# Performance work log

Measured on AMD Instinct MI355X. Metric: run time of the kernel, lower is better.

## Reference

```python
import jax, jax.numpy as jnp
import numpy as np
from jax import lax

M1 = M2 = M3 = 8  # Fourier modes per axis


def _corners(x):
    # gather the 4 low-frequency corner blocks -> [B, C, 2*M1, 2*M2, M3]
    top = jnp.concatenate([x[:, :, :M1, :M2, :M3], x[:, :, -M1:, :M2, :M3]], axis=2)
    bot = jnp.concatenate([x[:, :, :M1, -M2:, :M3], x[:, :, -M1:, -M2:, :M3]], axis=2)
    return jnp.concatenate([top, bot], axis=3)


def _scatter(template, xm):
    # place the mixed corner blocks back into a zero spectrum shaped like template
    xp = jnp.zeros_like(template)
    xp = xp.at[:, :, :M1, :M2, :M3].set(xm[:, :, :M1, :M2, :M3])
    xp = xp.at[:, :, -M1:, :M2, :M3].set(xm[:, :, -M1:, :M2, :M3])
    xp = xp.at[:, :, :M1, -M2:, :M3].set(xm[:, :, :M1, -M2:, :M3])
    xp = xp.at[:, :, -M1:, -M2:, :M3].set(xm[:, :, -M1:, -M2:, :M3])
    return xp


def _spectral_conv(x, w):
    # x: complex [B,C,X,Y,Zr]; w: real [Ci,Co,16,16,14]
    xm = _corners(x)                                    # [B,C,16,16,8] complex
    xr = jnp.fft.irfftn(xm, axes=(-3, -2, -1))          # [B,C,16,16,14] real
    y = jnp.einsum('bixyz,ioxyz->boxyz', xr, w)         # per-point channel mix
    ym = jnp.fft.rfftn(y, axes=(-3, -2, -1))            # [B,C,16,16,8] complex
    return _scatter(x, ym.astype(x.dtype))


def _cgelu(z):
    # torch: complex(gelu(real), gelu(imag)); F.gelu default is exact erf
    return lax.complex(jax.nn.gelu(z.real, approximate=False),
                       jax.nn.gelu(z.imag, approximate=False))


def _cmix(x, wr, wi):
    # einsum 'bi...,io...->bo...' with [Ci,Co,1,1,1] complex pointwise weight
    return jnp.einsum('bixyz,io->boxyz', x, lax.complex(wr, wi))


def setup_inputs() -> dict:
    key = jax.random.key(0)
    ks = jax.random.split(key, 12)
    B, X, Y, Zr = 4, 64, 64, 33
    W = 20
    inp = {
        'x_r': jax.random.normal(ks[0], (B, 3, X, Y, Zr), jnp.float32),
        'x_i': jax.random.normal(ks[1], (B, 3, X, Y, Zr), jnp.float32),
        'smooth': jax.random.uniform(ks[2], (1, 1, X, Y, Zr), jnp.float32),
        'wconv': 0.001 * jax.random.uniform(ks[3], (4, W, W, 2 * M1, 2 * M2, 2 * M3 - 2), jnp.float32),
        'wpt_r': 0.1 * jax.random.uniform(ks[4], (4, W, W), jnp.float32),
        'wpt_i': 0.1 * jax.random.uniform(ks[5], (4, W, W), jnp.float32),
        'fc0_r': 0.1 * jax.random.uniform(ks[6], (3, W), jnp.float32),
        'fc0_i': 0.1 * jax.random.uniform(ks[7], (3, W), jnp.float32),
        'fc1_r': 0.1 * jax.random.uniform(ks[8], (W, 128), jnp.float32),
        'fc1_i': 0.1 * jax.random.uniform(ks[9], (W, 128), jnp.float32),
        'fc2_r': 0.1 * jax.random.uniform(ks[10], (128, 3), jnp.float32),
        'fc2_i': 0.1 * jax.random.uniform(ks[11], (128, 3), jnp.float32),
    }
    return inp


def reference(x_r, x_i, smooth, wconv, wpt_r, wpt_i, fc0_r, fc0_i,
              fc1_r, fc1_i, fc2_r, fc2_i):
    x = lax.complex(x_r, x_i)                     # [B,3,64,64,33] complex64
    x = _cmix(x, fc0_r, fc0_i)                    # lift to width=20
    for l in range(4):
        x1 = _spectral_conv(x, wconv[l])
        x2 = _cmix(x, wpt_r[l], wpt_i[l])
        x = (x1 + x2) * smooth                    # real smoother broadcast
        if l < 3:
            x = _cgelu(x)
    x = _cmix(x, fc1_r, fc1_i)                    # 20 -> 128
    x = _cgelu(x)
    x = _cmix(x, fc2_r, fc2_i)                    # 128 -> 3
    return x
```

## Files before the change

### kernel.cpp

```cpp
#include <hip/hip_runtime.h>
#include <hip/hip_bf16.h>
#include <math.h>

#define XYZ 135168
#define W 20
#define NMODE 2048
#define NREAL 3584

__device__ __forceinline__ float n22_erf(float x) {
    float s = (x < 0.f) ? -1.f : 1.f;
    float a = fabsf(x);
    float t = 1.f / fmaf(0.3275911f, a, 1.f);
    float poly = t * fmaf(t, fmaf(t, fmaf(t, fmaf(t, 1.061405429f, -1.453152027f),
                                           1.421413741f), -0.284496736f), 0.254829592f);
    float e = __expf(-a * a);
    return s * (1.f - poly * e);
}
__device__ __forceinline__ float n22_gelu(float v) {
    return 0.5f * v * (1.0f + n22_erf(v * 0.7071067811865476f));
}

__global__ __launch_bounds__(256, 4)
void n22_fc0(const float* __restrict__ xr_in, const float* __restrict__ xi_in,
             const float* __restrict__ fr, const float* __restrict__ fi,
             float* __restrict__ xre, float* __restrict__ xim) {
    int idx = blockIdx.x * blockDim.x + threadIdx.x;
    if (idx >= 4 * XYZ) return;
    int b = idx / XYZ, p = idx % XYZ;
    float ar[3], ai[3];
#pragma unroll
    for (int i = 0; i < 3; i++) {
        ar[i] = xr_in[(size_t)(b * 3 + i) * XYZ + p];
        ai[i] = xi_in[(size_t)(b * 3 + i) * XYZ + p];
    }
#pragma unroll
    for (int o = 0; o < W; o++) {
        float rr = 0.f, ii = 0.f;
#pragma unroll
        for (int i = 0; i < 3; i++) {
            float wr = fr[i * W + o], wi = fi[i * W + o];
            rr += ar[i] * wr - ai[i] * wi;
            ii += ar[i] * wi + ai[i] * wr;
        }
        xre[(size_t)(b * W + o) * XYZ + p] = rr;
        xim[(size_t)(b * W + o) * XYZ + p] = ii;
    }
}

__global__ __launch_bounds__(256, 4)
void n22_ixy(const float* __restrict__ xre, const float* __restrict__ xim,
             float* __restrict__ aRe, float* __restrict__ aIm) {
    __shared__ float s0r[256], s0i[256], s1r[256], s1i[256];
    int bc = blockIdx.x >> 3;
    int kz = blockIdx.x & 7;
    int t = threadIdx.x;
    int hi = t >> 4, lo = t & 15;
    {
        int row = (hi < 8) ? hi : hi + 48;
        int col = (lo < 8) ? lo : lo + 48;
        int off = (row * 64 + col) * 33 + kz;
        s0r[t] = xre[(size_t)bc * XYZ + off];
        s0i[t] = xim[(size_t)bc * XYZ + off];
    }
    __syncthreads();
    {
        int nx = hi, ky = lo;
        float accr = 0.f, acci = 0.f;
        for (int kx = 0; kx < 16; kx++) {
            float vr = s0r[kx * 16 + ky], vi = s0i[kx * 16 + ky];
            int m = (kx * nx) & 15;
            float s, c;
            sincosf((float)m * 0.39269908169872414f, &s, &c);
            accr += vr * c - vi * s;
            acci += vr * s + vi * c;
        }
        s1r[t] = accr * 0.0625f;
        s1i[t] = acci * 0.0625f;
    }
    __syncthreads();
    {
        int nx = hi, ny = lo;
        float accr = 0.f, acci = 0.f;
        for (int ky = 0; ky < 16; ky++) {
            float vr = s1r[nx * 16 + ky], vi = s1i[nx * 16 + ky];
            int m = (ky * ny) & 15;
            float s, c;
            sincosf((float)m * 0.39269908169872414f, &s, &c);
            accr += vr * c - vi * s;
            acci += vr * s + vi * c;
        }
        size_t o = (size_t)bc * 2048 + (size_t)t * 8 + kz;
        aRe[o] = accr * 0.0625f;
        aIm[o] = acci * 0.0625f;
    }
}

__global__ __launch_bounds__(256, 4)
void n22_irfftz(const float* __restrict__ aRe, const float* __restrict__ aIm,
                float* __restrict__ r1) {
    int t = blockIdx.x * blockDim.x + threadIdx.x;
    if (t >= 80 * NREAL) return;
    int nz = t % 14;
    int q = t / 14;
    int base = q * 8;
    float acc = aRe[base];
    float re7 = aRe[base + 7];
    acc += (nz & 1) ? -re7 : re7;
    for (int k = 1; k < 7; k++) {
        int m = (k * nz) % 14;
        float s, c;
        sincosf((float)m * 0.4487989505128276f, &s, &c);
        acc += 2.f * (aRe[base + k] * c - aIm[base + k] * s);
    }
    r1[t] = acc * (1.0f / 14.0f);
}

__global__ __launch_bounds__(256, 4)
void n22_mix(const float* __restrict__ r1, const float* __restrict__ wconv,
             int l, float* __restrict__ r2) {
    int t = blockIdx.x * blockDim.x + threadIdx.x;
    if (t >= 80 * NREAL) return;
    int p = t % NREAL;
    int o = (t / NREAL) % W;
    int b = t / (NREAL * W);
    const float* wl = wconv + (size_t)l * W * W * NREAL;
    float acc = 0.f;
#pragma unroll
    for (int i = 0; i < W; i++)
        acc += r1[(size_t)(b * W + i) * NREAL + p] * wl[(size_t)(i * W + o) * NREAL + p];
    r2[t] = acc;
}

__global__ __launch_bounds__(256, 4)
void n22_rfftz(const float* __restrict__ r2,
               float* __restrict__ c1Re, float* __restrict__ c1Im) {
    int t = blockIdx.x * blockDim.x + threadIdx.x;
    if (t >= 80 * NMODE) return;
    int k = t & 7;
    int q = t >> 3;
    int base = q * 14;
    float accr = 0.f, acci = 0.f;
    for (int n = 0; n < 14; n++) {
        float v = r2[base + n];
        int m = (k * n) % 14;
        float s, c;
        sincosf((float)m * 0.4487989505128276f, &s, &c);
        accr += v * c;
        acci -= v * s;
    }
    c1Re[t] = accr;
    c1Im[t] = acci;
}

__global__ __launch_bounds__(256, 4)
void n22_fxy(const float* __restrict__ c1Re, const float* __restrict__ c1Im,
             float* __restrict__ eRe, float* __restrict__ eIm) {
    __shared__ float s0r[256], s0i[256], s1r[256], s1i[256];
    int bc = blockIdx.x >> 3;
    int kz = blockIdx.x & 7;
    int t = threadIdx.x;
    int hi = t >> 4, lo = t & 15;
    {
        size_t o = (size_t)bc * 2048 + (size_t)t * 8 + kz;
        s0r[t] = c1Re[o];
        s0i[t] = c1Im[o];
    }
    __syncthreads();
    {
        int kx = hi, ny = lo;
        float accr = 0.f, acci = 0.f;
        for (int nx = 0; nx < 16; nx++) {
            float vr = s0r[nx * 16 + ny], vi = s0i[nx * 16 + ny];
            int m = (kx * nx) & 15;
            float s, c;
            sincosf((float)m * 0.39269908169872414f, &s, &c);
            accr += vr * c + vi * s;
            acci += vi * c - vr * s;
        }
        s1r[t] = accr;
        s1i[t] = acci;
    }
    __syncthreads();
    {
        int kx = hi, ky = lo;
        float accr = 0.f, acci = 0.f;
        for (int ny = 0; ny < 16; ny++) {
            float vr = s1r[kx * 16 + ny], vi = s1i[kx * 16 + ny];
            int m = (ky * ny) & 15;
            float s, c;
            sincosf((float)m * 0.39269908169872414f, &s, &c);
            accr += vr * c + vi * s;
            acci += vi * c - vr * s;
        }
        size_t o = (size_t)bc * 2048 + (size_t)t * 8 + kz;
        eRe[o] = accr;
        eIm[o] = acci;
    }
}

__global__ __launch_bounds__(256, 4)
void n22_combine(float* __restrict__ xre, float* __restrict__ xim,
                 const float* __restrict__ ere, const float* __restrict__ eim,
                 const float* __restrict__ wpt_r, const float* __restrict__ wpt_i,
                 int l, const float* __restrict__ smooth) {
    __shared__ float wr[W * W], wi[W * W];
    for (int i = threadIdx.x; i < W * W; i += blockDim.x) {
        wr[i] = wpt_r[l * W * W + i];
        wi[i] = wpt_i[l * W * W + i];
    }
    __syncthreads();
    int idx = blockIdx.x * blockDim.x + threadIdx.x;
    if (idx >= 4 * XYZ) return;
    int b = idx / XYZ, p = idx % XYZ;
    int gz = p % 33;
    int gxy = p / 33;
    int gy = gxy & 63;
    int gx = gxy >> 6;
    int kx = (gx < 8) ? gx : ((gx >= 56) ? gx - 48 : -1);
    int ky = (gy < 8) ? gy : ((gy >= 56) ? gy - 48 : -1);
    bool corner = (kx >= 0) && (ky >= 0) && (gz < 8);
    float sm = smooth[p];
    float ar[W], ai[W];
#pragma unroll
    for (int i = 0; i < W; i++) {
        ar[i] = xre[(size_t)(b * W + i) * XYZ + p];
        ai[i] = xim[(size_t)(b * W + i) * XYZ + p];
    }
    int ebase = corner ? (b * W * NMODE + (kx * 16 + ky) * 8 + gz) : 0;
    for (int o = 0; o < W; o++) {
        float rr = 0.f, ii = 0.f;
#pragma unroll
        for (int i = 0; i < W; i++) {
            float wwr = wr[i * W + o], wwi = wi[i * W + o];
            rr += ar[i] * wwr - ai[i] * wwi;
            ii += ar[i] * wwi + ai[i] * wwr;
        }
        if (corner) {
            rr += ere[ebase + o * NMODE];
            ii += eim[ebase + o * NMODE];
        }
        rr *= sm;
        ii *= sm;
        rr = n22_gelu(rr);
        ii = n22_gelu(ii);
        xre[(size_t)(b * W + o) * XYZ + p] = rr;
        xim[(size_t)(b * W + o) * XYZ + p] = ii;
    }
}

__global__ __launch_bounds__(256, 2)
void n22_tail(const float* __restrict__ xre, const float* __restrict__ xim,
              const float* __restrict__ ere, const float* __restrict__ eim,
              const float* __restrict__ wpt_r, const float* __restrict__ wpt_i,
              const float* __restrict__ smooth,
              const float* __restrict__ f1r, const float* __restrict__ f1i,
              const float* __restrict__ f2r, const float* __restrict__ f2i,
              float* __restrict__ outf) {
    __shared__ __align__(16) float w1r[W * 128], w1i[W * 128];
    __shared__ __align__(16) float w2r[3 * 128], w2i[3 * 128];
    __shared__ float pwr[W * W], pwi[W * W];
    for (int i = threadIdx.x; i < W * 128; i += blockDim.x) {
        w1r[i] = f1r[i];
        w1i[i] = f1i[i];
    }
    for (int i = threadIdx.x; i < 3 * 128; i += blockDim.x) {
        int j = i & 127, o = i >> 7;
        w2r[o * 128 + j] = f2r[j * 3 + o];
        w2i[o * 128 + j] = f2i[j * 3 + o];
    }
    for (int i = threadIdx.x; i < W * W; i += blockDim.x) {
        pwr[i] = wpt_r[3 * W * W + i];
        pwi[i] = wpt_i[3 * W * W + i];
    }
    __syncthreads();
    int idx = blockIdx.x * blockDim.x + threadIdx.x;
    if (idx >= 4 * XYZ) return;
    int b = idx / XYZ, p = idx % XYZ;
    int gz = p % 33;
    int gxy = p / 33;
    int gy = gxy & 63;
    int gx = gxy >> 6;
    int kxc = (gx < 8) ? gx : ((gx >= 56) ? gx - 48 : -1);
    int kyc = (gy < 8) ? gy : ((gy >= 56) ? gy - 48 : -1);
    bool corner = (kxc >= 0) && (kyc >= 0) && (gz < 8);
    float sm = smooth[p];
    float rr_[W], ri_[W];
    {
        float ar[W], ai[W];
#pragma unroll
        for (int i = 0; i < W; i++) {
            ar[i] = xre[(size_t)(b * W + i) * XYZ + p];
            ai[i] = xim[(size_t)(b * W + i) * XYZ + p];
        }
        int ebase = corner ? (b * W * NMODE + (kxc * 16 + kyc) * 8 + gz) : 0;
#pragma unroll 1
        for (int o = 0; o < W; o++) {
            float rr = 0.f, ii = 0.f;
#pragma unroll
            for (int i = 0; i < W; i++) {
                float wwr = pwr[i * W + o], wwi = pwi[i * W + o];
                rr += ar[i] * wwr - ai[i] * wwi;
                ii += ar[i] * wwi + ai[i] * wwr;
            }
            if (corner) {
                rr += ere[ebase + o * NMODE];
                ii += eim[ebase + o * NMODE];
            }
            rr_[o] = rr * sm;
            ri_[o] = ii * sm;
        }
    }
    float accr[3] = {0.f, 0.f, 0.f};
    for (int jc = 0; jc < 16; jc++) {
        int jb = jc * 8;
        float tr[8], ti[8];
#pragma unroll
        for (int jj = 0; jj < 8; jj++) { tr[jj] = 0.f; ti[jj] = 0.f; }
#pragma unroll 1
        for (int i = 0; i < W; i++) {
            float4 wrA = *(const float4*)&w1r[i * 128 + jb];
            float4 wrB = *(const float4*)&w1r[i * 128 + jb + 4];
            float4 wiA = *(const float4*)&w1i[i * 128 + jb];
            float4 wiB = *(const float4*)&w1i[i * 128 + jb + 4];
            float xr_ = rr_[i], xi_ = ri_[i];
            tr[0] += xr_ * wrA.x - xi_ * wiA.x;  ti[0] += xr_ * wiA.x + xi_ * wrA.x;
            tr[1] += xr_ * wrA.y - xi_ * wiA.y;  ti[1] += xr_ * wiA.y + xi_ * wrA.y;
            tr[2] += xr_ * wrA.z - xi_ * wiA.z;  ti[2] += xr_ * wiA.z + xi_ * wrA.z;
            tr[3] += xr_ * wrA.w - xi_ * wiA.w;  ti[3] += xr_ * wiA.w + xi_ * wrA.w;
            tr[4] += xr_ * wrB.x - xi_ * wiB.x;  ti[4] += xr_ * wiB.x + xi_ * wrB.x;
            tr[5] += xr_ * wrB.y - xi_ * wiB.y;  ti[5] += xr_ * wiB.y + xi_ * wrB.y;
            tr[6] += xr_ * wrB.z - xi_ * wiB.z;  ti[6] += xr_ * wiB.z + xi_ * wrB.z;
            tr[7] += xr_ * wrB.w - xi_ * wiB.w;  ti[7] += xr_ * wiB.w + xi_ * wrB.w;
        }
#pragma unroll
        for (int jj = 0; jj < 8; jj++) {
            tr[jj] = n22_gelu(tr[jj]);
            ti[jj] = n22_gelu(ti[jj]);
        }
#pragma unroll
        for (int o = 0; o < 3; o++) {
            float4 crA = *(const float4*)&w2r[o * 128 + jb];
            float4 crB = *(const float4*)&w2r[o * 128 + jb + 4];
            float4 ciA = *(const float4*)&w2i[o * 128 + jb];
            float4 ciB = *(const float4*)&w2i[o * 128 + jb + 4];
            accr[o] += tr[0] * crA.x - ti[0] * ciA.x;
            accr[o] += tr[1] * crA.y - ti[1] * ciA.y;
            accr[o] += tr[2] * crA.z - ti[2] * ciA.z;
            accr[o] += tr[3] * crA.w - ti[3] * ciA.w;
            accr[o] += tr[4] * crB.x - ti[4] * ciB.x;
            accr[o] += tr[5] * crB.y - ti[5] * ciB.y;
            accr[o] += tr[6] * crB.z - ti[6] * ciB.z;
            accr[o] += tr[7] * crB.w - ti[7] * ciB.w;
        }
    }
#pragma unroll
    for (int o = 0; o < 3; o++) {
        size_t k = (size_t)(b * 3 + o) * XYZ + p;
        outf[k] = __bfloat162float(__float2bfloat16(accr[o]));
    }
}

extern "C" void kernel_launch(void* const* d_in, const int* in_sizes, int n_in,
                              void* d_out, int out_size, void* d_ws, size_t ws_size,
                              hipStream_t stream) {
    const float* x_r    = (const float*)d_in[0];
    const float* x_i    = (const float*)d_in[1];
    const float* smooth = (const float*)d_in[2];
    const float* wconv  = (const float*)d_in[3];
    const float* wpt_r  = (const float*)d_in[4];
    const float* wpt_i  = (const float*)d_in[5];
    const float* fc0_r  = (const float*)d_in[6];
    const float* fc0_i  = (const float*)d_in[7];
    const float* fc1_r  = (const float*)d_in[8];
    const float* fc1_i  = (const float*)d_in[9];
    const float* fc2_r  = (const float*)d_in[10];
    const float* fc2_i  = (const float*)d_in[11];
    float* outf = (float*)d_out;

    const size_t NBW = (size_t)4 * W * XYZ;
    const size_t NM  = (size_t)80 * NMODE;
    const size_t NR  = (size_t)80 * NREAL;

    float* ws  = (float*)d_ws;
    float* eRe = ws;
    float* eIm = eRe + NM;
    float* tRe = eIm + NM;
    float* tIm = tRe + NM;
    float* r1  = tIm + NM;
    float* r2  = r1 + NR;
    float* xre = r2 + NR;
    float* xim = xre + NBW;

    dim3 blk(256);
    const int gP = (4 * XYZ) / 256;
    const int gM = (80 * NMODE) / 256;
    const int gR = (80 * NREAL) / 256;

    n22_fc0<<<gP, blk, 0, stream>>>(x_r, x_i, fc0_r, fc0_i, xre, xim);
    for (int l = 0; l < 4; l++) {
        n22_ixy<<<640, blk, 0, stream>>>(xre, xim, tRe, tIm);
        n22_irfftz<<<gR, blk, 0, stream>>>(tRe, tIm, r1);
        n22_mix<<<gR, blk, 0, stream>>>(r1, wconv, l, r2);
        n22_rfftz<<<gM, blk, 0, stream>>>(r2, tRe, tIm);
        n22_fxy<<<640, blk, 0, stream>>>(tRe, tIm, eRe, eIm);
        if (l < 3)
            n22_combine<<<gP, blk, 0, stream>>>(xre, xim, eRe, eIm,
                                                wpt_r, wpt_i, l, smooth);
    }
    n22_tail<<<gP, blk, 0, stream>>>(xre, xim, eRe, eIm, wpt_r, wpt_i, smooth,
                                     fc1_r, fc1_i, fc2_r, fc2_i, outf);
}
```

Baseline: 729.1 us.

## Fuse z-axis irfft, channel mix and rfft into one shared-memory kernel

Merges the three per-layer kernels (inverse z DFT, pointwise channel mix, forward z DFT) into a single kernel that keeps the intermediates in LDS, so the r1/r2 buffers are never written to or read from global memory. Twiddle factors in the xy DFT kernels and the new fused kernel come from small shared tables instead of per-iteration sincosf calls. The tail kernel's launch bound changes from 2 to 4 waves. The fused kernel launches only 256 blocks, which may underfill the GPU, and the tighter tail bound can add register pressure.

```diff
diff --git a/kernel.cpp b/kernel.cpp
--- a/kernel.cpp
+++ b/kernel.cpp
@@ -7,7 +7,7 @@
 #define NMODE 2048
 #define NREAL 3584
 
-__device__ __forceinline__ float n22_erf(float x) {
+__device__ __forceinline__ float o23_erf(float x) {
     float s = (x < 0.f) ? -1.f : 1.f;
     float a = fabsf(x);
     float t = 1.f / fmaf(0.3275911f, a, 1.f);
@@ -16,12 +16,12 @@
     float e = __expf(-a * a);
     return s * (1.f - poly * e);
 }
-__device__ __forceinline__ float n22_gelu(float v) {
-    return 0.5f * v * (1.0f + n22_erf(v * 0.7071067811865476f));
-}
-
-__global__ __launch_bounds__(256, 4)
-void n22_fc0(const float* __restrict__ xr_in, const float* __restrict__ xi_in,
+__device__ __forceinline__ float o23_gelu(float v) {
+    return 0.5f * v * (1.0f + o23_erf(v * 0.7071067811865476f));
+}
+
+__global__ __launch_bounds__(256, 4)
+void o23_fc0(const float* __restrict__ xr_in, const float* __restrict__ xi_in,
              const float* __restrict__ fr, const float* __restrict__ fi,
              float* __restrict__ xre, float* __restrict__ xim) {
     int idx = blockIdx.x * blockDim.x + threadIdx.x;
@@ -48,13 +48,19 @@
 }
 
 __global__ __launch_bounds__(256, 4)
-void n22_ixy(const float* __restrict__ xre, const float* __restrict__ xim,
+void o23_ixy(const float* __restrict__ xre, const float* __restrict__ xim,
              float* __restrict__ aRe, float* __restrict__ aIm) {
     __shared__ float s0r[256], s0i[256], s1r[256], s1i[256];
+    __shared__ float twc[16], tws[16];
     int bc = blockIdx.x >> 3;
     int kz = blockIdx.x & 7;
     int t = threadIdx.x;
     int hi = t >> 4, lo = t & 15;
+    if (t < 16) {
+        float s, c;
+        sincosf((float)t * 0.39269908169872414f, &s, &c);
+        twc[t] = c; tws[t] = s;
+    }
     {
         int row = (hi < 8) ? hi : hi + 48;
         int col = (lo < 8) ? lo : lo + 48;
@@ -69,8 +75,7 @@
         for (int kx = 0; kx < 16; kx++) {
             float vr = s0r[kx * 16 + ky], vi = s0i[kx * 16 + ky];
             int m = (kx * nx) & 15;
-            float s, c;
-            sincosf((float)m * 0.39269908169872414f, &s, &c);
+            float c = twc[m], s = tws[m];
             accr += vr * c - vi * s;
             acci += vr * s + vi * c;
         }
@@ -84,8 +89,7 @@
         for (int ky = 0; ky < 16; ky++) {
             float vr = s1r[nx * 16 + ky], vi = s1i[nx * 16 + ky];
             int m = (ky * ny) & 15;
-            float s, c;
-            sincosf((float)m * 0.39269908169872414f, &s, &c);
+            float c = twc[m], s = tws[m];
             accr += vr * c - vi * s;
             acci += vr * s + vi * c;
         }
@@ -96,70 +100,91 @@
 }
 
 __global__ __launch_bounds__(256, 4)
-void n22_irfftz(const float* __restrict__ aRe, const float* __restrict__ aIm,
-                float* __restrict__ r1) {
-    int t = blockIdx.x * blockDim.x + threadIdx.x;
-    if (t >= 80 * NREAL) return;
-    int nz = t % 14;
-    int q = t / 14;
-    int base = q * 8;
-    float acc = aRe[base];
-    float re7 = aRe[base + 7];
-    acc += (nz & 1) ? -re7 : re7;
-    for (int k = 1; k < 7; k++) {
-        int m = (k * nz) % 14;
+void o23_zchain(const float* __restrict__ aRe, const float* __restrict__ aIm,
+                const float* __restrict__ wconv, int l,
+                float* __restrict__ tRe, float* __restrict__ tIm) {
+    __shared__ float sar[640], sai[640];
+    __shared__ float sr1[1120], sr2[1120];
+    __shared__ float twc[14], tws[14];
+    int b = blockIdx.x >> 6;
+    int q0 = (blockIdx.x & 63) * 4;
+    int tid = threadIdx.x;
+    if (tid < 14) {
         float s, c;
-        sincosf((float)m * 0.4487989505128276f, &s, &c);
-        acc += 2.f * (aRe[base + k] * c - aIm[base + k] * s);
-    }
-    r1[t] = acc * (1.0f / 14.0f);
-}
-
-__global__ __launch_bounds__(256, 4)
-void n22_mix(const float* __restrict__ r1, const float* __restrict__ wconv,
-             int l, float* __restrict__ r2) {
-    int t = blockIdx.x * blockDim.x + threadIdx.x;
-    if (t >= 80 * NREAL) return;
-    int p = t % NREAL;
-    int o = (t / NREAL) % W;
-    int b = t / (NREAL * W);
-    const float* wl = wconv + (size_t)l * W * W * NREAL;
-    float acc = 0.f;
-#pragma unroll
-    for (int i = 0; i < W; i++)
-        acc += r1[(size_t)(b * W + i) * NREAL + p] * wl[(size_t)(i * W + o) * NREAL + p];
-    r2[t] = acc;
-}
-
-__global__ __launch_bounds__(256, 4)
-void n22_rfftz(const float* __restrict__ r2,
-               float* __restrict__ c1Re, float* __restrict__ c1Im) {
-    int t = blockIdx.x * blockDim.x + threadIdx.x;
-    if (t >= 80 * NMODE) return;
-    int k = t & 7;
-    int q = t >> 3;
-    int base = q * 14;
-    float accr = 0.f, acci = 0.f;
-    for (int n = 0; n < 14; n++) {
-        float v = r2[base + n];
-        int m = (k * n) % 14;
-        float s, c;
-        sincosf((float)m * 0.4487989505128276f, &s, &c);
-        accr += v * c;
-        acci -= v * s;
-    }
-    c1Re[t] = accr;
-    c1Im[t] = acci;
-}
-
-__global__ __launch_bounds__(256, 4)
-void n22_fxy(const float* __restrict__ c1Re, const float* __restrict__ c1Im,
+        sincosf((float)tid * 0.4487989505128276f, &s, &c);
+        twc[tid] = c; tws[tid] = s;
+    }
+    for (int t = tid; t < 640; t += 256) {
+        int c = t >> 5;
+        int dq = (t >> 3) & 3;
+        int k = t & 7;
+        size_t g = (size_t)(b * 20 + c) * 2048 + (size_t)(q0 + dq) * 8 + k;
+        sar[t] = aRe[g];
+        sai[t] = aIm[g];
+    }
+    __syncthreads();
+    for (int t = tid; t < 1120; t += 256) {
+        int c = t / 56;
+        int rem = t % 56;
+        int dq = rem / 14, nz = rem % 14;
+        int base = c * 32 + dq * 8;
+        float acc = sar[base];
+        float re7 = sar[base + 7];
+        acc += (nz & 1) ? -re7 : re7;
+        for (int k = 1; k < 7; k++) {
+            int m = (k * nz) % 14;
+            acc += 2.f * (sar[base + k] * twc[m] - sai[base + k] * tws[m]);
+        }
+        sr1[t] = acc * (1.0f / 14.0f);
+    }
+    __syncthreads();
+    {
+        const float* wl = wconv + (size_t)l * W * W * NREAL;
+        for (int t = tid; t < 1120; t += 256) {
+            int o = t / 56;
+            int rem = t % 56;
+            int dq = rem / 14, nz = rem % 14;
+            int p = (q0 + dq) * 14 + nz;
+            float acc = 0.f;
+#pragma unroll 4
+            for (int i = 0; i < W; i++)
+                acc += sr1[i * 56 + rem] * wl[(size_t)(i * W + o) * NREAL + p];
+            sr2[t] = acc;
+        }
+    }
+    __syncthreads();
+    for (int t = tid; t < 640; t += 256) {
+        int c = t >> 5;
+        int dq = (t >> 3) & 3;
+        int k = t & 7;
+        int base = c * 56 + dq * 14;
+        float accr = 0.f, acci = 0.f;
+        for (int n = 0; n < 14; n++) {
+            float v = sr2[base + n];
+            int m = (k * n) % 14;
+            accr += v * twc[m];
+            acci -= v * tws[m];
+        }
+        size_t g = (size_t)(b * 20 + c) * 2048 + (size_t)(q0 + dq) * 8 + k;
+        tRe[g] = accr;
+        tIm[g] = acci;
+    }
+}
+
+__global__ __launch_bounds__(256, 4)
+void o23_fxy(const float* __restrict__ c1Re, const float* __restrict__ c1Im,
              float* __restrict__ eRe, float* __restrict__ eIm) {
     __shared__ float s0r[256], s0i[256], s1r[256], s1i[256];
+    __shared__ float twc[16], tws[16];
     int bc = blockIdx.x >> 3;
     int kz = blockIdx.x & 7;
     int t = threadIdx.x;
     int hi = t >> 4, lo = t & 15;
+    if (t < 16) {
+        float s, c;
+        sincosf((float)t * 0.39269908169872414f, &s, &c);
+        twc[t] = c; tws[t] = s;
+    }
     {
         size_t o = (size_t)bc * 2048 + (size_t)t * 8 + kz;
         s0r[t] = c1Re[o];
@@ -172,8 +197,7 @@
         for (int nx = 0; nx < 16; nx++) {
             float vr = s0r[nx * 16 + ny], vi = s0i[nx * 16 + ny];
             int m = (kx * nx) & 15;
-            float s, c;
-            sincosf((float)m * 0.39269908169872414f, &s, &c);
+            float c = twc[m], s = tws[m];
             accr += vr * c + vi * s;
             acci += vi * c - vr * s;
         }
@@ -187,8 +211,7 @@
         for (int ny = 0; ny < 16; ny++) {
             float vr = s1r[kx * 16 + ny], vi = s1i[kx * 16 + ny];
             int m = (ky * ny) & 15;
-            float s, c;
-            sincosf((float)m * 0.39269908169872414f, &s, &c);
+            float c = twc[m], s = tws[m];
             accr += vr * c + vi * s;
             acci += vi * c - vr * s;
         }
@@ -199,7 +222,7 @@
 }
 
 __global__ __launch_bounds__(256, 4)
-void n22_combine(float* __restrict__ xre, float* __restrict__ xim,
+void o23_combine(float* __restrict__ xre, float* __restrict__ xim,
                  const float* __restrict__ ere, const float* __restrict__ eim,
                  const float* __restrict__ wpt_r, const float* __restrict__ wpt_i,
                  int l, const float* __restrict__ smooth) {
@@ -241,15 +264,15 @@
         }
         rr *= sm;
         ii *= sm;
-        rr = n22_gelu(rr);
-        ii = n22_gelu(ii);
+        rr = o23_gelu(rr);
+        ii = o23_gelu(ii);
         xre[(size_t)(b * W + o) * XYZ + p] = rr;
         xim[(size_t)(b * W + o) * XYZ + p] = ii;
     }
 }
 
-__global__ __launch_bounds__(256, 2)
-void n22_tail(const float* __restrict__ xre, const float* __restrict__ xim,
+__global__ __launch_bounds__(256, 4)
+void o23_tail(const float* __restrict__ xre, const float* __restrict__ xim,
               const float* __restrict__ ere, const float* __restrict__ eim,
               const float* __restrict__ wpt_r, const float* __restrict__ wpt_i,
               const float* __restrict__ smooth,
@@ -334,8 +357,8 @@
         }
 #pragma unroll
         for (int jj = 0; jj < 8; jj++) {
-            tr[jj] = n22_gelu(tr[jj]);
-            ti[jj] = n22_gelu(ti[jj]);
+            tr[jj] = o23_gelu(tr[jj]);
+            ti[jj] = o23_gelu(ti[jj]);
         }
 #pragma unroll
         for (int o = 0; o < 3; o++) {
@@ -379,34 +402,27 @@
 
     const size_t NBW = (size_t)4 * W * XYZ;
     const size_t NM  = (size_t)80 * NMODE;
-    const size_t NR  = (size_t)80 * NREAL;
 
     float* ws  = (float*)d_ws;
     float* eRe = ws;
     float* eIm = eRe + NM;
     float* tRe = eIm + NM;
     float* tIm = tRe + NM;
-    float* r1  = tIm + NM;
-    float* r2  = r1 + NR;
-    float* xre = r2 + NR;
+    float* xre = tIm + NM;
     float* xim = xre + NBW;
 
     dim3 blk(256);
     const int gP = (4 * XYZ) / 256;
-    const int gM = (80 * NMODE) / 256;
-    const int gR = (80 * NREAL) / 256;
-
-    n22_fc0<<<gP, blk, 0, stream>>>(x_r, x_i, fc0_r, fc0_i, xre, xim);
+
+    o23_fc0<<<gP, blk, 0, stream>>>(x_r, x_i, fc0_r, fc0_i, xre, xim);
     for (int l = 0; l < 4; l++) {
-        n22_ixy<<<640, blk, 0, stream>>>(xre, xim, tRe, tIm);
-        n22_irfftz<<<gR, blk, 0, stream>>>(tRe, tIm, r1);
-        n22_mix<<<gR, blk, 0, stream>>>(r1, wconv, l, r2);
-        n22_rfftz<<<gM, blk, 0, stream>>>(r2, tRe, tIm);
-        n22_fxy<<<640, blk, 0, stream>>>(tRe, tIm, eRe, eIm);
+        o23_ixy<<<640, blk, 0, stream>>>(xre, xim, tRe, tIm);
+        o23_zchain<<<256, blk, 0, stream>>>(tRe, tIm, wconv, l, eRe, eIm);
+        o23_fxy<<<640, blk, 0, stream>>>(eRe, eIm, tRe, tIm);
         if (l < 3)
-            n22_combine<<<gP, blk, 0, stream>>>(xre, xim, eRe, eIm,
+            o23_combine<<<gP, blk, 0, stream>>>(xre, xim, tRe, tIm,
                                                 wpt_r, wpt_i, l, smooth);
     }
-    n22_tail<<<gP, blk, 0, stream>>>(xre, xim, eRe, eIm, wpt_r, wpt_i, smooth,
+    o23_tail<<<gP, blk, 0, stream>>>(xre, xim, tRe, tIm, wpt_r, wpt_i, smooth,
                                      fc1_r, fc1_i, fc2_r, fc2_i, outf);
 }
```

After: 751.1 us. 1.03x slower.
